# Kernel optimization log

Hardware: AMD Instinct MI355X
Metric: run time of the kernel (lower is better)

Reference implementation:

```python
import jax, jax.numpy as jnp
import numpy as np

TAL = 0.07
LOSS_WEIGHT = 1.0


def setup_inputs() -> dict:
    key = jax.random.key(0)
    k1, k2 = jax.random.split(key)
    feature = jax.random.normal(k1, (8192, 1024), dtype=jnp.float32)
    # labels all >= 1 so the foreground mask (label > 0) selects every row,
    # matching the original's fea = feature[label > 0] with a static shape.
    label = jax.random.randint(k2, (8192,), 1, 80, dtype=jnp.int32)
    return {"feature": feature, "label": label}


def reference(feature, label):
    # foreground=True and all labels > 0 -> fea = feature, lab = label
    fea = feature
    lab = label
    n = fea.shape[0]

    norm = jnp.linalg.norm(fea, axis=1)                      # [n]
    # ex[i, j] = <fea_i, fea_j> / (tal * ||fea_i|| * ||fea_j||)
    ex = (fea @ fea.T) / (TAL * norm[:, None] * norm[None, :])  # [n, n]

    # d_all = exp(ex); column sum pos_val + neg_val == sum_i d_all[i, j].
    # -log(d_all[i, j] / colsum_j) = logsumexp_i(ex[:, j]) - ex[i, j]
    log_colsum = jax.nn.logsumexp(ex, axis=0)                # [n]

    pos = lab[:, None] == lab[None, :]                       # pos[i, j]: lab_i == lab_j
    n_pos = jnp.sum(pos, axis=0).astype(ex.dtype)            # per-anchor positive count

    per_pair = jnp.where(pos, log_colsum[None, :] - ex, jnp.zeros((), ex.dtype))
    loss_anc = jnp.sum(per_pair, axis=0) / n_pos             # [n], mean over positives
    loss = jnp.sum(loss_anc)
    return LOSS_WEIGHT * loss / n
```

## Files before the change

kernel.cpp:

```cpp
#include <hip/hip_runtime.h>

#define TAL 0.07f
constexpr int N = 8192;
constexpr int D = 1024;
constexpr int NB = 64;
constexpr int NTILES = NB * (NB + 1) / 2;
constexpr int TPX = NTILES / 8;

typedef __bf16 bf16x8 __attribute__((ext_vector_type(8)));
typedef float f32x4 __attribute__((ext_vector_type(4)));

#define AS1 __attribute__((address_space(1)))
#define AS3 __attribute__((address_space(3)))

static __device__ __forceinline__ ushort f2bf(float x) {
    union { float f; uint32_t u; } c; c.f = x;
    uint32_t u = c.u;
    uint32_t r = (u + 0x7FFFu + ((u >> 16) & 1u)) >> 16;
    return (ushort)r;
}

__global__ __launch_bounds__(256) void prep_kernel(const float* __restrict__ F,
                                                   ushort* __restrict__ Fb,
                                                   float* __restrict__ ascale) {
    int row = blockIdx.x * 4 + (threadIdx.x >> 6);
    int lane = threadIdx.x & 63;
    const float4* src = (const float4*)(F + (size_t)row * D);
    ushort4* dst = (ushort4*)(Fb + (size_t)row * D);
    float local = 0.f;
    #pragma unroll
    for (int it = 0; it < 4; ++it) {
        float4 v = src[it * 64 + lane];
        ushort4 o;
        o.x = f2bf(v.x); o.y = f2bf(v.y); o.z = f2bf(v.z); o.w = f2bf(v.w);
        dst[it * 64 + lane] = o;
        local += v.x*v.x + v.y*v.y + v.z*v.z + v.w*v.w;
    }
    #pragma unroll
    for (int off = 32; off; off >>= 1) local += __shfl_xor(local, off);
    if (lane == 0) ascale[row] = rsqrtf(TAL * local);
}

__global__ void hist_kernel(const int* __restrict__ lab, int* __restrict__ hist) {
    int i = blockIdx.x * blockDim.x + threadIdx.x;
    if (i < N) atomicAdd(&hist[lab[i]], 1);
}

#define BM 128
#define BN 128
#define BK 32
#define TILE (BM * BK)
#define NSTEP (D / BK)

__global__ __launch_bounds__(256, 4) void gemm_kernel(const ushort* __restrict__ Fb,
                                                      const float* __restrict__ ascale,
                                                      const int* __restrict__ lab,
                                                      float* __restrict__ gSumE,
                                                      float* __restrict__ gSumP) {
    __shared__ ushort sA[2][TILE];
    __shared__ ushort sB[2][TILE];
    __shared__ float rScale[BM], cScale[BN];
    __shared__ int rLab[BM], cLab[BN];

    int k = blockIdx.x;
    int b = (k & 7) * TPX + (k >> 3);

    int bi = (int)((sqrtf(8.f * (float)b + 1.f) - 1.f) * 0.5f);
    while ((bi + 1) * (bi + 2) / 2 <= b) ++bi;
    while (bi * (bi + 1) / 2 > b) --bi;
    int bj = b - bi * (bi + 1) / 2;
    bool offdiag = (bi != bj);

    int I0 = bi * BM, J0 = bj * BN;
    int t = threadIdx.x;
    int lane = t & 63, w = t >> 6;
    int wr = w >> 1, wc = w & 1;

    if (t < 128) { rScale[t] = ascale[I0 + t]; rLab[t] = lab[I0 + t]; }
    else { int u = t - 128; cScale[u] = ascale[J0 + u]; cLab[u] = lab[J0 + u]; }

    f32x4 acc[4][4];
    #pragma unroll
    for (int m = 0; m < 4; ++m)
        #pragma unroll
        for (int n = 0; n < 4; ++n)
            acc[m][n] = {0.f, 0.f, 0.f, 0.f};

    int r0 = (w * 2 + 0) * 16 + (lane >> 2);
    int r1 = (w * 2 + 1) * 16 + (lane >> 2);
    int ce = (lane & 3) * 8;
    const ushort* srcA0 = Fb + (size_t)(I0 + r0) * D + ce;
    const ushort* srcA1 = Fb + (size_t)(I0 + r1) * D + ce;
    const ushort* srcB0 = Fb + (size_t)(J0 + r0) * D + ce;
    const ushort* srcB1 = Fb + (size_t)(J0 + r1) * D + ce;
    ushort* sAf = &sA[0][0];
    ushort* sBf = &sB[0][0];
    int d0 = (w * 2 + 0) * 512;
    int d1 = (w * 2 + 1) * 512;

#define STAGE(c, koff) do {                                                                              \
    __builtin_amdgcn_global_load_lds((const AS1 void*)(srcA0 + (koff)), (AS3 void*)(sAf + (c)*TILE + d0), 16, 0, 0); \
    __builtin_amdgcn_global_load_lds((const AS1 void*)(srcA1 + (koff)), (AS3 void*)(sAf + (c)*TILE + d1), 16, 0, 0); \
    __builtin_amdgcn_global_load_lds((const AS1 void*)(srcB0 + (koff)), (AS3 void*)(sBf + (c)*TILE + d0), 16, 0, 0); \
    __builtin_amdgcn_global_load_lds((const AS1 void*)(srcB1 + (koff)), (AS3 void*)(sBf + (c)*TILE + d1), 16, 0, 0); \
} while (0)

    int kb = (lane >> 4) * 8;
    int fr = lane & 15;

    STAGE(0, 0);
    __syncthreads();

    int cur = 0;
    for (int step = 0; step < NSTEP; ++step) {
        if (step + 1 < NSTEP) STAGE(cur ^ 1, (step + 1) * BK);

        const ushort* a = sAf + cur * TILE;
        const ushort* bb = sBf + cur * TILE;
        bf16x8 af[4], bfr[4];
        #pragma unroll
        for (int m = 0; m < 4; ++m)
            af[m] = *(const bf16x8*)(a + (wr * 64 + m * 16 + fr) * BK + kb);
        #pragma unroll
        for (int n = 0; n < 4; ++n)
            bfr[n] = *(const bf16x8*)(bb + (wc * 64 + n * 16 + fr) * BK + kb);
        #pragma unroll
        for (int m = 0; m < 4; ++m)
            #pragma unroll
            for (int n = 0; n < 4; ++n)
                acc[m][n] = __builtin_amdgcn_mfma_f32_16x16x32_bf16(af[m], bfr[n], acc[m][n], 0, 0, 0);

        if (step + 1 < NSTEP) __syncthreads();
        cur ^= 1;
    }

    float rs[16]; int rl[16];
    int rbase = wr * 64 + (lane >> 4) * 4;
    #pragma unroll
    for (int m = 0; m < 4; ++m)
        #pragma unroll
        for (int r = 0; r < 4; ++r) {
            rs[m * 4 + r] = rScale[rbase + m * 16 + r];
            rl[m * 4 + r] = rLab[rbase + m * 16 + r];
        }

    const float CSH = 1.0f / TAL;
    float colE[4], colP[4], rowE[16], rowP[16];
    #pragma unroll
    for (int n = 0; n < 4; ++n) { colE[n] = 0.f; colP[n] = 0.f; }
    #pragma unroll
    for (int q = 0; q < 16; ++q) { rowE[q] = 0.f; rowP[q] = 0.f; }

    #pragma unroll
    for (int n = 0; n < 4; ++n) {
        int jl = wc * 64 + n * 16 + fr;
        float aj = cScale[jl];
        int lj = cLab[jl];
        #pragma unroll
        for (int m = 0; m < 4; ++m)
            #pragma unroll
            for (int r = 0; r < 4; ++r) {
                float ex = acc[m][n][r] * rs[m * 4 + r] * aj;
                float e = __expf(ex - CSH);
                float p = (rl[m * 4 + r] == lj) ? ex : 0.f;
                colE[n] += e; colP[n] += p;
                rowE[m * 4 + r] += e; rowP[m * 4 + r] += p;
            }
    }

    #pragma unroll
    for (int n = 0; n < 4; ++n) {
        float se = colE[n], sp = colP[n];
        se += __shfl_xor(se, 16); se += __shfl_xor(se, 32);
        sp += __shfl_xor(sp, 16); sp += __shfl_xor(sp, 32);
        if (lane < 16) {
            int jl = wc * 64 + n * 16 + lane;
            atomicAdd(&gSumE[J0 + jl], se);
            atomicAdd(&gSumP[J0 + jl], sp);
        }
    }

    if (offdiag) {
        #pragma unroll
        for (int q = 0; q < 16; ++q) {
            float se = rowE[q], sp = rowP[q];
            se += __shfl_xor(se, 1); se += __shfl_xor(se, 2);
            se += __shfl_xor(se, 4); se += __shfl_xor(se, 8);
            sp += __shfl_xor(sp, 1); sp += __shfl_xor(sp, 2);
            sp += __shfl_xor(sp, 4); sp += __shfl_xor(sp, 8);
            if ((lane & 15) == 0) {
                int row = rbase + (q >> 2) * 16 + (q & 3);
                atomicAdd(&gSumE[I0 + row], se);
                atomicAdd(&gSumP[I0 + row], sp);
            }
        }
    }
}

__global__ __launch_bounds__(256) void finalize_kernel(const float* __restrict__ gSumE,
                                                       const float* __restrict__ gSumP,
                                                       const int* __restrict__ lab,
                                                       const int* __restrict__ hist,
                                                       float* __restrict__ out) {
    int t = threadIdx.x;
    const float CSH = 1.0f / TAL;
    float local = 0.f;
    for (int j = t; j < N; j += 256) {
        float np = (float)hist[lab[j]];
        local += CSH + logf(gSumE[j]) - gSumP[j] / np;
    }
    #pragma unroll
    for (int off = 32; off; off >>= 1) local += __shfl_xor(local, off);
    __shared__ float red[4];
    if ((t & 63) == 0) red[t >> 6] = local;
    __syncthreads();
    if (t == 0) out[0] = (red[0] + red[1] + red[2] + red[3]) / (float)N;
}

extern "C" void kernel_launch(void* const* d_in, const int* in_sizes, int n_in,
                              void* d_out, int out_size, void* d_ws, size_t ws_size,
                              hipStream_t stream) {
    const float* F = (const float*)d_in[0];
    const int* lab = (const int*)d_in[1];
    float* out = (float*)d_out;
    char* ws = (char*)d_ws;

    const size_t FB_BYTES = (size_t)N * D * 2;
    ushort* Fb    = (ushort*)ws;
    float* ascale = (float*)(ws + FB_BYTES);
    float* gSumE  = (float*)(ws + FB_BYTES + 32768);
    float* gSumP  = (float*)(ws + FB_BYTES + 65536);
    int*   hist   = (int*)  (ws + FB_BYTES + 98304);

    hipMemsetAsync(ws + FB_BYTES + 32768, 0, 65536 + 512, stream);

    prep_kernel<<<N / 4, 256, 0, stream>>>(F, Fb, ascale);
    hist_kernel<<<N / 256, 256, 0, stream>>>(lab, hist);
    gemm_kernel<<<NTILES, 256, 0, stream>>>(Fb, ascale, lab, gSumE, gSumP);
    finalize_kernel<<<1, 256, 0, stream>>>(gSumE, gSumP, lab, hist, out);
}
```

Measured before the change: 242.3 us.

## Triple-buffer GEMM loads with swizzled LDS and fuse histogram into prep

The GEMM main loop now uses a three-stage LDS ring with explicit vmcnt/lgkmcnt waits and raw barriers, so global loads run two steps ahead of the MFMA compute. LDS reads and writes use an XOR swizzle on the k-chunk to reduce bank conflicts. The label histogram moves into the prep kernel, removing one launch. The extra LDS buffer lowers the occupancy target from 4 to 3 blocks per CU, and the hand-placed waits add correctness risk.

```diff
diff --git a/kernel.cpp b/kernel.cpp
--- a/kernel.cpp
+++ b/kernel.cpp
@@ -13,6 +13,11 @@
 #define AS1 __attribute__((address_space(1)))
 #define AS3 __attribute__((address_space(3)))
 
+#define WAIT_VM(n) asm volatile("s_waitcnt vmcnt(" #n ")" ::: "memory")
+#define WAIT_LGKM0 asm volatile("s_waitcnt lgkmcnt(0)" ::: "memory")
+#define SCHED_FENCE __builtin_amdgcn_sched_barrier(0)
+#define SBAR __builtin_amdgcn_s_barrier()
+
 static __device__ __forceinline__ ushort f2bf(float x) {
     union { float f; uint32_t u; } c; c.f = x;
     uint32_t u = c.u;
@@ -21,8 +26,10 @@
 }
 
 __global__ __launch_bounds__(256) void prep_kernel(const float* __restrict__ F,
+                                                   const int* __restrict__ lab,
                                                    ushort* __restrict__ Fb,
-                                                   float* __restrict__ ascale) {
+                                                   float* __restrict__ ascale,
+                                                   int* __restrict__ hist) {
     int row = blockIdx.x * 4 + (threadIdx.x >> 6);
     int lane = threadIdx.x & 63;
     const float4* src = (const float4*)(F + (size_t)row * D);
@@ -38,12 +45,10 @@
     }
     #pragma unroll
     for (int off = 32; off; off >>= 1) local += __shfl_xor(local, off);
-    if (lane == 0) ascale[row] = rsqrtf(TAL * local);
-}
-
-__global__ void hist_kernel(const int* __restrict__ lab, int* __restrict__ hist) {
-    int i = blockIdx.x * blockDim.x + threadIdx.x;
-    if (i < N) atomicAdd(&hist[lab[i]], 1);
+    if (lane == 0) {
+        ascale[row] = rsqrtf(TAL * local);
+        atomicAdd(&hist[lab[row]], 1);
+    }
 }
 
 #define BM 128
@@ -52,18 +57,18 @@
 #define TILE (BM * BK)
 #define NSTEP (D / BK)
 
-__global__ __launch_bounds__(256, 4) void gemm_kernel(const ushort* __restrict__ Fb,
+__global__ __launch_bounds__(256, 3) void gemm_kernel(const ushort* __restrict__ Fb,
                                                       const float* __restrict__ ascale,
                                                       const int* __restrict__ lab,
                                                       float* __restrict__ gSumE,
                                                       float* __restrict__ gSumP) {
-    __shared__ ushort sA[2][TILE];
-    __shared__ ushort sB[2][TILE];
+    __shared__ ushort sA[3][TILE];
+    __shared__ ushort sB[3][TILE];
     __shared__ float rScale[BM], cScale[BN];
     __shared__ int rLab[BM], cLab[BN];
 
-    int k = blockIdx.x;
-    int b = (k & 7) * TPX + (k >> 3);
+    int kblk = blockIdx.x;
+    int b = (kblk & 7) * TPX + (kblk >> 3);
 
     int bi = (int)((sqrtf(8.f * (float)b + 1.f) - 1.f) * 0.5f);
     while ((bi + 1) * (bi + 2) / 2 <= b) ++bi;
@@ -88,7 +93,7 @@
 
     int r0 = (w * 2 + 0) * 16 + (lane >> 2);
     int r1 = (w * 2 + 1) * 16 + (lane >> 2);
-    int ce = (lane & 3) * 8;
+    int ce = (((lane & 3) ^ ((lane >> 3) & 3))) * 8;
     const ushort* srcA0 = Fb + (size_t)(I0 + r0) * D + ce;
     const ushort* srcA1 = Fb + (size_t)(I0 + r1) * D + ce;
     const ushort* srcB0 = Fb + (size_t)(J0 + r0) * D + ce;
@@ -105,34 +110,47 @@
     __builtin_amdgcn_global_load_lds((const AS1 void*)(srcB1 + (koff)), (AS3 void*)(sBf + (c)*TILE + d1), 16, 0, 0); \
 } while (0)
 
-    int kb = (lane >> 4) * 8;
     int fr = lane & 15;
-
-    STAGE(0, 0);
+    int cs = ((lane >> 4) ^ ((lane >> 1) & 3)) * 8;
+
+#define COMPUTE(cb, SECOND_BAR) do {                                                   \
+    const ushort* a_ = sAf + (cb) * TILE;                                              \
+    const ushort* b_ = sBf + (cb) * TILE;                                              \
+    bf16x8 af[4], bfr[4];                                                              \
+    _Pragma("unroll")                                                                  \
+    for (int m = 0; m < 4; ++m)                                                        \
+        af[m] = *(const bf16x8*)(a_ + (wr * 64 + m * 16 + fr) * BK + cs);              \
+    _Pragma("unroll")                                                                  \
+    for (int n = 0; n < 4; ++n)                                                        \
+        bfr[n] = *(const bf16x8*)(b_ + (wc * 64 + n * 16 + fr) * BK + cs);             \
+    WAIT_LGKM0; SCHED_FENCE;                                                           \
+    if (SECOND_BAR) { SBAR; SCHED_FENCE; }                                             \
+    _Pragma("unroll")                                                                  \
+    for (int m = 0; m < 4; ++m)                                                        \
+        _Pragma("unroll")                                                              \
+        for (int n = 0; n < 4; ++n)                                                    \
+            acc[m][n] = __builtin_amdgcn_mfma_f32_16x16x32_bf16(af[m], bfr[n], acc[m][n], 0, 0, 0); \
+} while (0)
+
+#define ITER(cb, sb, tt) do {                                                          \
+    STAGE(sb, ((tt) + 2) * BK);                                                        \
+    WAIT_VM(8); SCHED_FENCE; SBAR; SCHED_FENCE;                                        \
+    COMPUTE(cb, 1);                                                                    \
+} while (0)
+
+    STAGE(0, 0 * BK);
+    STAGE(1, 1 * BK);
     __syncthreads();
 
-    int cur = 0;
-    for (int step = 0; step < NSTEP; ++step) {
-        if (step + 1 < NSTEP) STAGE(cur ^ 1, (step + 1) * BK);
-
-        const ushort* a = sAf + cur * TILE;
-        const ushort* bb = sBf + cur * TILE;
-        bf16x8 af[4], bfr[4];
-        #pragma unroll
-        for (int m = 0; m < 4; ++m)
-            af[m] = *(const bf16x8*)(a + (wr * 64 + m * 16 + fr) * BK + kb);
-        #pragma unroll
-        for (int n = 0; n < 4; ++n)
-            bfr[n] = *(const bf16x8*)(bb + (wc * 64 + n * 16 + fr) * BK + kb);
-        #pragma unroll
-        for (int m = 0; m < 4; ++m)
-            #pragma unroll
-            for (int n = 0; n < 4; ++n)
-                acc[m][n] = __builtin_amdgcn_mfma_f32_16x16x32_bf16(af[m], bfr[n], acc[m][n], 0, 0, 0);
-
-        if (step + 1 < NSTEP) __syncthreads();
-        cur ^= 1;
-    }
+    for (int s = 0; s < NSTEP - 2; s += 3) {
+        ITER(0, 2, s);
+        ITER(1, 0, s + 1);
+        ITER(2, 1, s + 2);
+    }
+    WAIT_VM(4); SCHED_FENCE; SBAR; SCHED_FENCE;
+    COMPUTE(0, 0);
+    WAIT_VM(0); SCHED_FENCE; SBAR; SCHED_FENCE;
+    COMPUTE(1, 0);
 
     float rs[16]; int rl[16];
     int rbase = wr * 64 + (lane >> 4) * 4;
@@ -234,8 +252,7 @@
 
     hipMemsetAsync(ws + FB_BYTES + 32768, 0, 65536 + 512, stream);
 
-    prep_kernel<<<N / 4, 256, 0, stream>>>(F, Fb, ascale);
-    hist_kernel<<<N / 256, 256, 0, stream>>>(lab, hist);
+    prep_kernel<<<N / 4, 256, 0, stream>>>(F, lab, Fb, ascale, hist);
     gemm_kernel<<<NTILES, 256, 0, stream>>>(Fb, ascale, lab, gSumE, gSumP);
     finalize_kernel<<<1, 256, 0, stream>>>(gSumE, gSumP, lab, hist, out);
 }
```

After: 246.4 us. About the same (+1.7%).
